# Kernel optimization log

Measured on AMD Instinct MI355X. Metric: run time of the kernel, lower is better.

Reference implementation:

```python
import jax, jax.numpy as jnp
import numpy as np

N_NODES = 100000
N_EDGES = 3200000
N_GRAPHS = 512


def setup_inputs() -> dict:
    key = jax.random.key(0)
    k1, k2, k3, k4, k5 = jax.random.split(key, 5)
    x = jax.random.normal(k1, (N_NODES, 5), dtype=jnp.float32)
    edge_index = jax.random.randint(k2, (2, N_EDGES), 0, N_NODES, dtype=jnp.int64)
    batch = jnp.sort(jax.random.randint(k3, (N_NODES,), 0, N_GRAPHS, dtype=jnp.int64))
    W1 = jax.random.normal(k4, (5, 16), dtype=jnp.float32) * (1.0 / np.sqrt(5.0))
    b1 = jnp.zeros((16,), dtype=jnp.float32)
    W2 = jax.random.normal(k5, (16, 16), dtype=jnp.float32) * 0.25
    b2 = jnp.zeros((16,), dtype=jnp.float32)
    return {"x": x, "edge_index": edge_index, "batch": batch,
            "W1": W1, "b1": b1, "W2": W2, "b2": b2}


def _gcn_conv(x, src, dst, norm, W, b, n_nodes):
    # PyG GCNConv: h = X W; out_i = sum_{j->i} norm_ij * h_j + b
    h = x @ W                                   # [N, out]
    msgs = h[src] * norm[:, None]               # gather + scale  [E_tot, out]
    out = jax.ops.segment_sum(msgs, dst, num_segments=n_nodes)
    return out + b


def reference(x, edge_index, batch, W1, b1, W2, b2):
    n = x.shape[0]
    # add self-loops (GCNConv default)
    loops = jnp.arange(n, dtype=edge_index.dtype)
    src = jnp.concatenate([edge_index[0], loops])
    dst = jnp.concatenate([edge_index[1], loops])
    # symmetric normalization: deg computed on destination nodes
    deg = jax.ops.segment_sum(jnp.ones_like(src, dtype=x.dtype), dst, num_segments=n)
    dinv = jnp.where(deg > 0, jax.lax.rsqrt(deg), 0.0)
    norm = dinv[src] * dinv[dst]                # [E_tot]

    h = jax.nn.relu(_gcn_conv(x, src, dst, norm, W1, b1, n))
    h = jax.nn.relu(_gcn_conv(h, src, dst, norm, W2, b2, n))

    # global mean pool over graphs in the batch
    sums = jax.ops.segment_sum(h, batch, num_segments=N_GRAPHS)
    cnts = jax.ops.segment_sum(jnp.ones((n,), dtype=h.dtype), batch, num_segments=N_GRAPHS)
    return sums / jnp.maximum(cnts, 1.0)[:, None]
```

## Files before the change

### kernel.cpp

```cpp
#include <hip/hip_runtime.h>

#define N_NODES  100000
#define N_EDGES  3200000
#define N_GRAPHS 512
#define F_IN     5
#define F_HID    16

#define PBLK   512
#define CHUNK  4096
#define NBLK   ((N_EDGES + CHUNK - 1) / CHUNK)
#define BKT_NODES 256
#define NBKT ((N_NODES + BKT_NODES - 1) / BKT_NODES)
#define HPAD   512
#define CAP    10240


__device__ inline unsigned short f2bf(float f) {
    unsigned u = __float_as_uint(f);
    return (unsigned short)((u + 0x7fffu + ((u >> 16) & 1u)) >> 16);
}
__device__ inline float bf2f(unsigned short h) {
    return __uint_as_float(((unsigned)h) << 16);
}
__device__ inline void unpack16(uint4 r0, uint4 r1, float* f) {
    f[0]  = bf2f((unsigned short)r0.x); f[1]  = bf2f((unsigned short)(r0.x >> 16));
    f[2]  = bf2f((unsigned short)r0.y); f[3]  = bf2f((unsigned short)(r0.y >> 16));
    f[4]  = bf2f((unsigned short)r0.z); f[5]  = bf2f((unsigned short)(r0.z >> 16));
    f[6]  = bf2f((unsigned short)r0.w); f[7]  = bf2f((unsigned short)(r0.w >> 16));
    f[8]  = bf2f((unsigned short)r1.x); f[9]  = bf2f((unsigned short)(r1.x >> 16));
    f[10] = bf2f((unsigned short)r1.y); f[11] = bf2f((unsigned short)(r1.y >> 16));
    f[12] = bf2f((unsigned short)r1.z); f[13] = bf2f((unsigned short)(r1.z >> 16));
    f[14] = bf2f((unsigned short)r1.w); f[15] = bf2f((unsigned short)(r1.w >> 16));
}

template <int NW>
__device__ inline int block_incl_scan(int v, int t, int* wsum) {
    int lane = t & 63, wave = t >> 6;
    int x = v;
#pragma unroll
    for (int o = 1; o < 64; o <<= 1) {
        int y = __shfl_up(x, o, 64);
        if (lane >= o) x += y;
    }
    if (lane == 63) wsum[wave] = x;
    __syncthreads();
    if (t < 64) {
        int w = (t < NW) ? wsum[t] : 0;
#pragma unroll
        for (int o = 1; o < NW; o <<= 1) {
            int y = __shfl_up(w, o, 64);
            if (t >= o) w += y;
        }
        if (t < NW) wsum[t] = w;
    }
    __syncthreads();
    return x + (wave ? wsum[wave - 1] : 0);
}


__global__ void k_zero(float* __restrict__ out, float* __restrict__ cnt) {
    int i = blockIdx.x * blockDim.x + threadIdx.x;
    if (i < N_GRAPHS * F_HID) out[i] = 0.0f;
    if (i < N_GRAPHS) cnt[i] = 0.0f;
}

__global__ __launch_bounds__(PBLK) void k_count(const int* __restrict__ dst,
                                                const int* __restrict__ batch,
                                                int* __restrict__ H,
                                                float* __restrict__ cnt) {
    __shared__ int hist[HPAD];
    __shared__ int bcnt[8];
    __shared__ int g0s;
    int t = threadIdx.x, blk = blockIdx.x;
    int chunk0 = blk * CHUNK;
    int n4 = min(CHUNK, N_EDGES - chunk0) >> 2;
    hist[t] = 0;
    if (t < 8) bcnt[t] = 0;
    if (t == 0 && blk < NBKT) {
        int nb = blk * BKT_NODES;
        g0s = batch[nb < N_NODES ? nb : N_NODES - 1];
    }
    __syncthreads();
    const int4* d4 = (const int4*)(dst + chunk0);
#pragma unroll
    for (int i = 0; i < CHUNK / 4 / PBLK; i++) {
        int k = t + i * PBLK;
        if (k < n4) {
            int4 d = d4[k];
            atomicAdd(&hist[d.x >> 8], 1);
            atomicAdd(&hist[d.y >> 8], 1);
            atomicAdd(&hist[d.z >> 8], 1);
            atomicAdd(&hist[d.w >> 8], 1);
        }
    }
    if (blk < NBKT && t < BKT_NODES) {
        int i2 = blk * BKT_NODES + t;
        if (i2 < N_NODES) {
            int g = batch[i2];
            int l = g - g0s;
            if (l >= 0 && l < 8) atomicAdd(&bcnt[l], 1);
            else atomicAdd(&cnt[g], 1.0f);
        }
    }
    __syncthreads();
    H[blk * HPAD + t] = hist[t];
    if (blk < NBKT && t < 8 && bcnt[t] > 0) atomicAdd(&cnt[g0s + t], (float)bcnt[t]);
}

__global__ __launch_bounds__(256) void k_scan(int* __restrict__ H,
                                              int* __restrict__ cnt_b) {
    __shared__ int wsum[8];
    int b = blockIdx.x, t = threadIdx.x;
    int v[4];
    int s = 0;
#pragma unroll
    for (int i = 0; i < 4; i++) {
        int pos = t * 4 + i;
        v[i] = (pos < NBLK) ? H[pos * HPAD + b] : 0;
        s += v[i];
    }
    int incl = block_incl_scan<4>(s, t, wsum);
    int run = incl - s;
#pragma unroll
    for (int i = 0; i < 4; i++) {
        int pos = t * 4 + i;
        if (pos < NBLK) H[pos * HPAD + b] = run;
        run += v[i];
    }
    if (t == 255) cnt_b[b] = incl;
}

__global__ __launch_bounds__(PBLK) void k_scatter(const int* __restrict__ src,
                                                  const int* __restrict__ dst,
                                                  const int* __restrict__ H,
                                                  unsigned* __restrict__ packed) {
    __shared__ int hist[HPAD];
    __shared__ int scn[HPAD];
    __shared__ int rnk[HPAD];
    __shared__ int base[HPAD];
    __shared__ int wsum[8];
    __shared__ unsigned pkd[CHUNK];
    __shared__ unsigned short bkt[CHUNK];
    int t = threadIdx.x, blk = blockIdx.x;
    int chunk0 = blk * CHUNK;
    int n = min(CHUNK, N_EDGES - chunk0);
    int n4 = n >> 2;
    hist[t] = 0;
    base[t] = H[blk * HPAD + t];
    __syncthreads();
    const int4* s4 = (const int4*)(src + chunk0);
    const int4* d4 = (const int4*)(dst + chunk0);
    int4 lsv[CHUNK / 4 / PBLK], ldv[CHUNK / 4 / PBLK];
#pragma unroll
    for (int i = 0; i < CHUNK / 4 / PBLK; i++) {
        int k = t + i * PBLK;
        if (k < n4) {
            lsv[i] = s4[k];
            ldv[i] = d4[k];
            atomicAdd(&hist[ldv[i].x >> 8], 1);
            atomicAdd(&hist[ldv[i].y >> 8], 1);
            atomicAdd(&hist[ldv[i].z >> 8], 1);
            atomicAdd(&hist[ldv[i].w >> 8], 1);
        }
    }
    __syncthreads();
    int v = hist[t];
    int incl = block_incl_scan<8>(v, t, wsum);
    int excl = incl - v;
    scn[t] = excl;
    rnk[t] = excl;
    __syncthreads();
#pragma unroll
    for (int i = 0; i < CHUNK / 4 / PBLK; i++) {
        int k = t + i * PBLK;
        if (k < n4) {
            int ds0 = ldv[i].x, ds1 = ldv[i].y, ds2 = ldv[i].z, ds3 = ldv[i].w;
            int ss0 = lsv[i].x, ss1 = lsv[i].y, ss2 = lsv[i].z, ss3 = lsv[i].w;
            int b0 = ds0 >> 8, b1 = ds1 >> 8, b2 = ds2 >> 8, b3 = ds3 >> 8;
            int r0 = atomicAdd(&rnk[b0], 1);
            pkd[r0] = ((unsigned)ss0 << 8) | (unsigned)(ds0 & 255);
            bkt[r0] = (unsigned short)b0;
            int r1 = atomicAdd(&rnk[b1], 1);
            pkd[r1] = ((unsigned)ss1 << 8) | (unsigned)(ds1 & 255);
            bkt[r1] = (unsigned short)b1;
            int r2 = atomicAdd(&rnk[b2], 1);
            pkd[r2] = ((unsigned)ss2 << 8) | (unsigned)(ds2 & 255);
            bkt[r2] = (unsigned short)b2;
            int r3 = atomicAdd(&rnk[b3], 1);
            pkd[r3] = ((unsigned)ss3 << 8) | (unsigned)(ds3 & 255);
            bkt[r3] = (unsigned short)b3;
        }
    }
    __syncthreads();
    for (int p = t; p < n; p += PBLK) {
        int b = bkt[p];
        packed[(size_t)b * CAP + base[b] + (p - scn[b])] = pkd[p];
    }
}

__global__ __launch_bounds__(1024) void k_deg(const int* __restrict__ cnt_b,
                                              const unsigned* __restrict__ packed,
                                              const float* __restrict__ x,
                                              const float* __restrict__ W1,
                                              float* __restrict__ dinv,
                                              unsigned short* __restrict__ pb) {
    __shared__ int hist[BKT_NODES];
    __shared__ float w1[F_IN * F_HID];
    __shared__ int tots;
    int b = blockIdx.x, t = threadIdx.x;
    if (t < BKT_NODES) hist[t] = 0;
    if (t >= 256 && t < 256 + F_IN * F_HID) w1[t - 256] = W1[t - 256];
    if (t == 0) tots = min(cnt_b[b], CAP);
    __syncthreads();
    int tot = tots;
    const unsigned* pk = packed + (size_t)b * CAP;
    for (int k = t; k < tot; k += 1024)
        atomicAdd(&hist[pk[k] & 255], 1);
    __syncthreads();
    if (t < BKT_NODES) {
        int node = b * BKT_NODES + t;
        if (node < N_NODES) {
            float di = rsqrtf((float)(1 + hist[t]));
            dinv[node] = di;
            float xi[F_IN];
#pragma unroll
            for (int k = 0; k < F_IN; k++) xi[k] = x[node * F_IN + k];
            unsigned pkk[8];
#pragma unroll
            for (int q = 0; q < 8; q++) {
                float h0 = 0.0f, h1 = 0.0f;
#pragma unroll
                for (int k = 0; k < F_IN; k++) {
                    h0 += xi[k] * w1[k * F_HID + 2 * q];
                    h1 += xi[k] * w1[k * F_HID + 2 * q + 1];
                }
                pkk[q] = (unsigned)f2bf(h0 * di) | ((unsigned)f2bf(h1 * di) << 16);
            }
            uint4* d4 = (uint4*)(pb + (size_t)node * F_HID);
            d4[0] = make_uint4(pkk[0], pkk[1], pkk[2], pkk[3]);
            d4[1] = make_uint4(pkk[4], pkk[5], pkk[6], pkk[7]);
        }
    }
}

__global__ __launch_bounds__(1024) void k_agg1(const int* __restrict__ cnt_b,
                                               const unsigned* __restrict__ packed,
                                               const unsigned short* __restrict__ pb,
                                               const float* __restrict__ dinv,
                                               const float* __restrict__ W2,
                                               const float* __restrict__ b1,
                                               unsigned short* __restrict__ pb2) {
    __shared__ int hist[BKT_NODES];
    __shared__ int beg[BKT_NODES];
    __shared__ int rnk[BKT_NODES];
    __shared__ int wsum[16];
    __shared__ float w2[F_HID * F_HID];
    __shared__ float b1s[F_HID];
    __shared__ int colL[CAP];
    __shared__ int tots;
    int b = blockIdx.x, t = threadIdx.x;
    const uint4* pb16 = (const uint4*)pb;
    if (t < BKT_NODES) hist[t] = 0;
    if (t >= 256 && t < 512) w2[t - 256] = W2[t - 256];
    if (t >= 512 && t < 512 + F_HID) b1s[t - 512] = b1[t - 512];
    if (t == 0) tots = min(cnt_b[b], CAP);
    __syncthreads();
    int tot = tots;
    const unsigned* pk = packed + (size_t)b * CAP;
    for (int k = t; k < tot; k += 1024)
        atomicAdd(&hist[pk[k] & 255], 1);
    __syncthreads();
    int v = (t < BKT_NODES) ? hist[t] : 0;
    int incl = block_incl_scan<16>(v, t, wsum);
    if (t < BKT_NODES) { beg[t] = incl - v; rnk[t] = incl - v; }
    __syncthreads();
    for (int k = t; k < tot; k += 1024) {
        unsigned u = pk[k];
        int r = atomicAdd(&rnk[u & 255], 1);
        colL[r] = (int)(u >> 8);
    }
    __syncthreads();
    int nl = t >> 2, q = t & 3;
    int node = b * BKT_NODES + nl;
    float f[F_HID];
    if (node < N_NODES && q == 0) {
        unpack16(pb16[node * 2], pb16[node * 2 + 1], f);
    } else {
#pragma unroll
        for (int c = 0; c < F_HID; c++) f[c] = 0.0f;
    }
    if (node < N_NODES) {
        int b0 = beg[nl], len = hist[nl];
        for (int i = q; i < len; i += 4) {
            int s = colL[b0 + i];
            uint4 r0 = pb16[s * 2], r1 = pb16[s * 2 + 1];
            float g[F_HID];
            unpack16(r0, r1, g);
#pragma unroll
            for (int c = 0; c < F_HID; c++) f[c] += g[c];
        }
    }
#pragma unroll
    for (int c = 0; c < F_HID; c++) {
        f[c] += __shfl_xor(f[c], 1, 64);
        f[c] += __shfl_xor(f[c], 2, 64);
    }
    if (node < N_NODES) {
        float di = dinv[node];
        float h[F_HID];
#pragma unroll
        for (int c = 0; c < F_HID; c++)
            h[c] = fmaxf(di * f[c] + b1s[c], 0.0f);
        float m0 = 0.0f, m1 = 0.0f, m2 = 0.0f, m3 = 0.0f;
#pragma unroll
        for (int c = 0; c < F_HID; c++) {
            float4 wv = *(const float4*)&w2[c * F_HID + 4 * q];
            m0 += h[c] * wv.x; m1 += h[c] * wv.y; m2 += h[c] * wv.z; m3 += h[c] * wv.w;
        }
        unsigned p0 = (unsigned)f2bf(m0 * di) | ((unsigned)f2bf(m1 * di) << 16);
        unsigned p1 = (unsigned)f2bf(m2 * di) | ((unsigned)f2bf(m3 * di) << 16);
        *(uint2*)(pb2 + (size_t)node * F_HID + 4 * q) = make_uint2(p0, p1);
    }
}

__global__ __launch_bounds__(1024) void k_agg2(const int* __restrict__ cnt_b,
                                               const unsigned* __restrict__ packed,
                                               const unsigned short* __restrict__ pb,
                                               const float* __restrict__ dinv,
                                               const int* __restrict__ batch,
                                               const float* __restrict__ b2,
                                               const float* __restrict__ cnt,
                                               float* __restrict__ out) {
    __shared__ int hist[BKT_NODES];
    __shared__ int beg[BKT_NODES];
    __shared__ int rnk[BKT_NODES];
    __shared__ int wsum[16];
    __shared__ float b2s[F_HID];
    __shared__ float accT[F_HID][BKT_NODES];
    __shared__ int bl[BKT_NODES];
    __shared__ int colL[CAP];
    __shared__ int tots;
    int b = blockIdx.x, t = threadIdx.x;
    const uint4* pb16 = (const uint4*)pb;
    if (t < BKT_NODES) {
        hist[t] = 0;
        int nn = b * BKT_NODES + t;
        bl[t] = (nn < N_NODES) ? batch[nn] : -1;
    }
    if (t >= 512 && t < 512 + F_HID) b2s[t - 512] = b2[t - 512];
    if (t == 0) tots = min(cnt_b[b], CAP);
    __syncthreads();
    int tot = tots;
    const unsigned* pk = packed + (size_t)b * CAP;
    for (int k = t; k < tot; k += 1024)
        atomicAdd(&hist[pk[k] & 255], 1);
    __syncthreads();
    int v = (t < BKT_NODES) ? hist[t] : 0;
    int incl = block_incl_scan<16>(v, t, wsum);
    if (t < BKT_NODES) { beg[t] = incl - v; rnk[t] = incl - v; }
    __syncthreads();
    for (int k = t; k < tot; k += 1024) {
        unsigned u = pk[k];
        int r = atomicAdd(&rnk[u & 255], 1);
        colL[r] = (int)(u >> 8);
    }
    __syncthreads();
    int nl = t >> 2, q = t & 3;
    int node = b * BKT_NODES + nl;
    float f[F_HID];
    if (node < N_NODES && q == 0) {
        unpack16(pb16[node * 2], pb16[node * 2 + 1], f);
    } else {
#pragma unroll
        for (int c = 0; c < F_HID; c++) f[c] = 0.0f;
    }
    if (node < N_NODES) {
        int b0 = beg[nl], len = hist[nl];
        for (int i = q; i < len; i += 4) {
            int s = colL[b0 + i];
            uint4 r0 = pb16[s * 2], r1 = pb16[s * 2 + 1];
            float g[F_HID];
            unpack16(r0, r1, g);
#pragma unroll
            for (int c = 0; c < F_HID; c++) f[c] += g[c];
        }
    }
#pragma unroll
    for (int c = 0; c < F_HID; c++) {
        f[c] += __shfl_xor(f[c], 1, 64);
        f[c] += __shfl_xor(f[c], 2, 64);
    }
    if (node < N_NODES) {
        float di = dinv[node];
#pragma unroll
        for (int e = 0; e < 4; e++) {
            int c = 4 * q + e;
            accT[c][nl] = fmaxf(di * f[c] + b2s[c], 0.0f);
        }
    }
    __syncthreads();
    if (t < 256) {
        int l = t >> 4, ch = t & 15;
        int g = bl[0] + l;
        if (g < N_GRAPHS) {
            float s = 0.0f;
            int m = 0;
            for (int n0 = 0; n0 < 256; n0++) {
                int n = (n0 + ch + 16 * l) & 255;
                if (bl[n] == g) { s += accT[ch][n]; m++; }
            }
            if (m > 0) atomicAdd(&out[g * F_HID + ch], s / cnt[g]);
        }
    }
}


extern "C" void kernel_launch(void* const* d_in, const int* in_sizes, int n_in,
                              void* d_out, int out_size, void* d_ws, size_t ws_size,
                              hipStream_t stream) {
    const float* x     = (const float*)d_in[0];
    const int*   ei    = (const int*)d_in[1];
    const int*   batch = (const int*)d_in[2];
    const float* W1    = (const float*)d_in[3];
    const float* b1    = (const float*)d_in[4];
    const float* W2    = (const float*)d_in[5];
    const float* b2    = (const float*)d_in[6];
    float* out = (float*)d_out;

    int*            H      = (int*)d_ws;
    int*            cnt_b  = H + (size_t)NBLK * HPAD;
    unsigned*       packed = (unsigned*)(cnt_b + 512);
    float*          dinv   = (float*)(packed + (size_t)NBKT * CAP);
    unsigned short* pb_a   = (unsigned short*)(dinv + N_NODES);
    unsigned short* pb_b   = pb_a + (size_t)N_NODES * F_HID;
    float*          cnt    = (float*)(pb_b + (size_t)N_NODES * F_HID);

    const int* src = ei;
    const int* dst = ei + N_EDGES;

    k_zero<<<(N_GRAPHS * F_HID + 255) / 256, 256, 0, stream>>>(out, cnt);
    k_count<<<NBLK, PBLK, 0, stream>>>(dst, batch, H, cnt);
    k_scan<<<NBKT, 256, 0, stream>>>(H, cnt_b);
    k_scatter<<<NBLK, PBLK, 0, stream>>>(src, dst, H, packed);
    k_deg<<<NBKT, 1024, 0, stream>>>(cnt_b, packed, x, W1, dinv, pb_a);
    k_agg1<<<NBKT, 1024, 0, stream>>>(cnt_b, packed, pb_a, dinv, W2, b1, pb_b);
    k_agg2<<<NBKT, 1024, 0, stream>>>(cnt_b, packed, pb_b, dinv, batch, b2, cnt, out);
}
```

Baseline: 187.2 us.

## Replace bucketed shared-memory sort with global-atomic CSR build and per-node pull

Replaces the two-level bucket sort (per-chunk shared histograms, transposed scan, bucket scatter, then a per-bucket local re-sort in every aggregation kernel) with a direct CSR build: global atomic degree count, three-stage scan to row offsets, and a fill pass using global atomic cursors. The aggregation kernels then read the CSR column array directly in small 256-thread blocks instead of re-sorting each bucket in shared memory twice. This removes the repeated per-layer local sort and its large shared memory footprint, but adds heavy global atomic traffic (two passes of 3.2M random atomics) and writes edges in a scattered, nondeterministic order within each row.

```diff
diff --git a/kernel.cpp b/kernel.cpp
--- a/kernel.cpp
+++ b/kernel.cpp
@@ -6,13 +6,11 @@
 #define F_IN     5
 #define F_HID    16
 
-#define PBLK   512
-#define CHUNK  4096
-#define NBLK   ((N_EDGES + CHUNK - 1) / CHUNK)
-#define BKT_NODES 256
-#define NBKT ((N_NODES + BKT_NODES - 1) / BKT_NODES)
-#define HPAD   512
-#define CAP    10240
+#define NB256  ((N_NODES + 255) / 256)
+#define EBLK   2048
+#define NEB    ((N_EDGES + EBLK - 1) / EBLK)
+#define PN     64
+#define NPB    ((N_NODES + PN - 1) / PN)
 
 
 __device__ inline unsigned short f2bf(float f) {
@@ -58,242 +56,161 @@
 }
 
 
-__global__ void k_zero(float* __restrict__ out, float* __restrict__ cnt) {
-    int i = blockIdx.x * blockDim.x + threadIdx.x;
+__global__ __launch_bounds__(256) void k_zero(int* __restrict__ deg,
+                                              float* __restrict__ out,
+                                              float* __restrict__ cnt) {
+    int i = blockIdx.x * 256 + threadIdx.x;
+    if (i < N_NODES) deg[i] = 0;
     if (i < N_GRAPHS * F_HID) out[i] = 0.0f;
     if (i < N_GRAPHS) cnt[i] = 0.0f;
 }
 
-__global__ __launch_bounds__(PBLK) void k_count(const int* __restrict__ dst,
-                                                const int* __restrict__ batch,
-                                                int* __restrict__ H,
-                                                float* __restrict__ cnt) {
-    __shared__ int hist[HPAD];
+__global__ __launch_bounds__(256) void k_deg0(const int* __restrict__ dst,
+                                              int* __restrict__ deg) {
+    int t = threadIdx.x, blk = blockIdx.x;
+    int c0 = blk * EBLK;
+    int n4 = min(EBLK, N_EDGES - c0) >> 2;
+    const int4* d4 = (const int4*)(dst + c0);
+#pragma unroll
+    for (int i = 0; i < EBLK / 4 / 256; i++) {
+        int k = t + i * 256;
+        if (k < n4) {
+            int4 d = d4[k];
+            atomicAdd(&deg[d.x], 1);
+            atomicAdd(&deg[d.y], 1);
+            atomicAdd(&deg[d.z], 1);
+            atomicAdd(&deg[d.w], 1);
+        }
+    }
+}
+
+__global__ __launch_bounds__(256) void k_scanA(const int* __restrict__ deg,
+                                               const int* __restrict__ batch,
+                                               int* __restrict__ S,
+                                               float* __restrict__ cnt) {
+    __shared__ int wsum[4];
     __shared__ int bcnt[8];
     __shared__ int g0s;
+    int b = blockIdx.x, t = threadIdx.x;
+    int node = b * 256 + t;
+    if (t < 8) bcnt[t] = 0;
+    if (t == 0) g0s = batch[(b * 256) < N_NODES ? (b * 256) : N_NODES - 1];
+    __syncthreads();
+    int v = (node < N_NODES) ? deg[node] : 0;
+    int lane = t & 63, wave = t >> 6;
+    int x = v;
+#pragma unroll
+    for (int o = 1; o < 64; o <<= 1) x += __shfl_xor(x, o, 64);
+    if (lane == 0) wsum[wave] = x;
+    if (node < N_NODES) {
+        int g = batch[node];
+        int l = g - g0s;
+        if (l >= 0 && l < 8) atomicAdd(&bcnt[l], 1);
+        else atomicAdd(&cnt[g], 1.0f);
+    }
+    __syncthreads();
+    if (t == 0) S[b] = wsum[0] + wsum[1] + wsum[2] + wsum[3];
+    if (t < 8 && bcnt[t] > 0) atomicAdd(&cnt[g0s + t], (float)bcnt[t]);
+}
+
+__global__ __launch_bounds__(512) void k_scanB(const int* __restrict__ S,
+                                               int* __restrict__ Boff) {
+    __shared__ int wsum[8];
+    int t = threadIdx.x;
+    int v = (t < NB256) ? S[t] : 0;
+    int incl = block_incl_scan<8>(v, t, wsum);
+    if (t < NB256) Boff[t] = incl - v;
+}
+
+__global__ __launch_bounds__(256) void k_scanC(const int* __restrict__ deg,
+                                               const int* __restrict__ Boff,
+                                               const float* __restrict__ x,
+                                               const float* __restrict__ W1,
+                                               int2* __restrict__ rowbc,
+                                               int* __restrict__ cur,
+                                               float* __restrict__ dinv,
+                                               unsigned short* __restrict__ pb) {
+    __shared__ int wsum[4];
+    __shared__ float w1[F_IN * F_HID];
+    int b = blockIdx.x, t = threadIdx.x;
+    if (t < F_IN * F_HID) w1[t] = W1[t];
+    int node = b * 256 + t;
+    int v = (node < N_NODES) ? deg[node] : 0;
+    int incl = block_incl_scan<4>(v, t, wsum);
+    int beg = Boff[b] + incl - v;
+    if (node < N_NODES) {
+        rowbc[node] = make_int2(beg, v);
+        cur[node] = beg;
+        float di = rsqrtf((float)(1 + v));
+        dinv[node] = di;
+        float xi[F_IN];
+#pragma unroll
+        for (int k = 0; k < F_IN; k++) xi[k] = x[node * F_IN + k];
+        unsigned pkk[8];
+#pragma unroll
+        for (int q = 0; q < 8; q++) {
+            float h0 = 0.0f, h1 = 0.0f;
+#pragma unroll
+            for (int k = 0; k < F_IN; k++) {
+                h0 += xi[k] * w1[k * F_HID + 2 * q];
+                h1 += xi[k] * w1[k * F_HID + 2 * q + 1];
+            }
+            pkk[q] = (unsigned)f2bf(h0 * di) | ((unsigned)f2bf(h1 * di) << 16);
+        }
+        uint4* d4 = (uint4*)(pb + (size_t)node * F_HID);
+        d4[0] = make_uint4(pkk[0], pkk[1], pkk[2], pkk[3]);
+        d4[1] = make_uint4(pkk[4], pkk[5], pkk[6], pkk[7]);
+    }
+}
+
+__global__ __launch_bounds__(256) void k_fill(const int* __restrict__ src,
+                                              const int* __restrict__ dst,
+                                              int* __restrict__ cur,
+                                              int* __restrict__ col) {
     int t = threadIdx.x, blk = blockIdx.x;
-    int chunk0 = blk * CHUNK;
-    int n4 = min(CHUNK, N_EDGES - chunk0) >> 2;
-    hist[t] = 0;
-    if (t < 8) bcnt[t] = 0;
-    if (t == 0 && blk < NBKT) {
-        int nb = blk * BKT_NODES;
-        g0s = batch[nb < N_NODES ? nb : N_NODES - 1];
-    }
-    __syncthreads();
-    const int4* d4 = (const int4*)(dst + chunk0);
-#pragma unroll
-    for (int i = 0; i < CHUNK / 4 / PBLK; i++) {
-        int k = t + i * PBLK;
+    int c0 = blk * EBLK;
+    int n4 = min(EBLK, N_EDGES - c0) >> 2;
+    const int4* s4 = (const int4*)(src + c0);
+    const int4* d4 = (const int4*)(dst + c0);
+#pragma unroll
+    for (int i = 0; i < EBLK / 4 / 256; i++) {
+        int k = t + i * 256;
         if (k < n4) {
-            int4 d = d4[k];
-            atomicAdd(&hist[d.x >> 8], 1);
-            atomicAdd(&hist[d.y >> 8], 1);
-            atomicAdd(&hist[d.z >> 8], 1);
-            atomicAdd(&hist[d.w >> 8], 1);
-        }
-    }
-    if (blk < NBKT && t < BKT_NODES) {
-        int i2 = blk * BKT_NODES + t;
-        if (i2 < N_NODES) {
-            int g = batch[i2];
-            int l = g - g0s;
-            if (l >= 0 && l < 8) atomicAdd(&bcnt[l], 1);
-            else atomicAdd(&cnt[g], 1.0f);
-        }
-    }
-    __syncthreads();
-    H[blk * HPAD + t] = hist[t];
-    if (blk < NBKT && t < 8 && bcnt[t] > 0) atomicAdd(&cnt[g0s + t], (float)bcnt[t]);
-}
-
-__global__ __launch_bounds__(256) void k_scan(int* __restrict__ H,
-                                              int* __restrict__ cnt_b) {
-    __shared__ int wsum[8];
-    int b = blockIdx.x, t = threadIdx.x;
-    int v[4];
-    int s = 0;
-#pragma unroll
-    for (int i = 0; i < 4; i++) {
-        int pos = t * 4 + i;
-        v[i] = (pos < NBLK) ? H[pos * HPAD + b] : 0;
-        s += v[i];
-    }
-    int incl = block_incl_scan<4>(s, t, wsum);
-    int run = incl - s;
-#pragma unroll
-    for (int i = 0; i < 4; i++) {
-        int pos = t * 4 + i;
-        if (pos < NBLK) H[pos * HPAD + b] = run;
-        run += v[i];
-    }
-    if (t == 255) cnt_b[b] = incl;
-}
-
-__global__ __launch_bounds__(PBLK) void k_scatter(const int* __restrict__ src,
-                                                  const int* __restrict__ dst,
-                                                  const int* __restrict__ H,
-                                                  unsigned* __restrict__ packed) {
-    __shared__ int hist[HPAD];
-    __shared__ int scn[HPAD];
-    __shared__ int rnk[HPAD];
-    __shared__ int base[HPAD];
-    __shared__ int wsum[8];
-    __shared__ unsigned pkd[CHUNK];
-    __shared__ unsigned short bkt[CHUNK];
-    int t = threadIdx.x, blk = blockIdx.x;
-    int chunk0 = blk * CHUNK;
-    int n = min(CHUNK, N_EDGES - chunk0);
-    int n4 = n >> 2;
-    hist[t] = 0;
-    base[t] = H[blk * HPAD + t];
-    __syncthreads();
-    const int4* s4 = (const int4*)(src + chunk0);
-    const int4* d4 = (const int4*)(dst + chunk0);
-    int4 lsv[CHUNK / 4 / PBLK], ldv[CHUNK / 4 / PBLK];
-#pragma unroll
-    for (int i = 0; i < CHUNK / 4 / PBLK; i++) {
-        int k = t + i * PBLK;
-        if (k < n4) {
-            lsv[i] = s4[k];
-            ldv[i] = d4[k];
-            atomicAdd(&hist[ldv[i].x >> 8], 1);
-            atomicAdd(&hist[ldv[i].y >> 8], 1);
-            atomicAdd(&hist[ldv[i].z >> 8], 1);
-            atomicAdd(&hist[ldv[i].w >> 8], 1);
-        }
-    }
-    __syncthreads();
-    int v = hist[t];
-    int incl = block_incl_scan<8>(v, t, wsum);
-    int excl = incl - v;
-    scn[t] = excl;
-    rnk[t] = excl;
-    __syncthreads();
-#pragma unroll
-    for (int i = 0; i < CHUNK / 4 / PBLK; i++) {
-        int k = t + i * PBLK;
-        if (k < n4) {
-            int ds0 = ldv[i].x, ds1 = ldv[i].y, ds2 = ldv[i].z, ds3 = ldv[i].w;
-            int ss0 = lsv[i].x, ss1 = lsv[i].y, ss2 = lsv[i].z, ss3 = lsv[i].w;
-            int b0 = ds0 >> 8, b1 = ds1 >> 8, b2 = ds2 >> 8, b3 = ds3 >> 8;
-            int r0 = atomicAdd(&rnk[b0], 1);
-            pkd[r0] = ((unsigned)ss0 << 8) | (unsigned)(ds0 & 255);
-            bkt[r0] = (unsigned short)b0;
-            int r1 = atomicAdd(&rnk[b1], 1);
-            pkd[r1] = ((unsigned)ss1 << 8) | (unsigned)(ds1 & 255);
-            bkt[r1] = (unsigned short)b1;
-            int r2 = atomicAdd(&rnk[b2], 1);
-            pkd[r2] = ((unsigned)ss2 << 8) | (unsigned)(ds2 & 255);
-            bkt[r2] = (unsigned short)b2;
-            int r3 = atomicAdd(&rnk[b3], 1);
-            pkd[r3] = ((unsigned)ss3 << 8) | (unsigned)(ds3 & 255);
-            bkt[r3] = (unsigned short)b3;
-        }
-    }
-    __syncthreads();
-    for (int p = t; p < n; p += PBLK) {
-        int b = bkt[p];
-        packed[(size_t)b * CAP + base[b] + (p - scn[b])] = pkd[p];
-    }
-}
-
-__global__ __launch_bounds__(1024) void k_deg(const int* __restrict__ cnt_b,
-                                              const unsigned* __restrict__ packed,
-                                              const float* __restrict__ x,
-                                              const float* __restrict__ W1,
-                                              float* __restrict__ dinv,
-                                              unsigned short* __restrict__ pb) {
-    __shared__ int hist[BKT_NODES];
-    __shared__ float w1[F_IN * F_HID];
-    __shared__ int tots;
-    int b = blockIdx.x, t = threadIdx.x;
-    if (t < BKT_NODES) hist[t] = 0;
-    if (t >= 256 && t < 256 + F_IN * F_HID) w1[t - 256] = W1[t - 256];
-    if (t == 0) tots = min(cnt_b[b], CAP);
-    __syncthreads();
-    int tot = tots;
-    const unsigned* pk = packed + (size_t)b * CAP;
-    for (int k = t; k < tot; k += 1024)
-        atomicAdd(&hist[pk[k] & 255], 1);
-    __syncthreads();
-    if (t < BKT_NODES) {
-        int node = b * BKT_NODES + t;
-        if (node < N_NODES) {
-            float di = rsqrtf((float)(1 + hist[t]));
-            dinv[node] = di;
-            float xi[F_IN];
-#pragma unroll
-            for (int k = 0; k < F_IN; k++) xi[k] = x[node * F_IN + k];
-            unsigned pkk[8];
-#pragma unroll
-            for (int q = 0; q < 8; q++) {
-                float h0 = 0.0f, h1 = 0.0f;
-#pragma unroll
-                for (int k = 0; k < F_IN; k++) {
-                    h0 += xi[k] * w1[k * F_HID + 2 * q];
-                    h1 += xi[k] * w1[k * F_HID + 2 * q + 1];
-                }
-                pkk[q] = (unsigned)f2bf(h0 * di) | ((unsigned)f2bf(h1 * di) << 16);
-            }
-            uint4* d4 = (uint4*)(pb + (size_t)node * F_HID);
-            d4[0] = make_uint4(pkk[0], pkk[1], pkk[2], pkk[3]);
-            d4[1] = make_uint4(pkk[4], pkk[5], pkk[6], pkk[7]);
-        }
-    }
-}
-
-__global__ __launch_bounds__(1024) void k_agg1(const int* __restrict__ cnt_b,
-                                               const unsigned* __restrict__ packed,
+            int4 s = s4[k], d = d4[k];
+            int r0 = atomicAdd(&cur[d.x], 1); col[r0] = s.x;
+            int r1 = atomicAdd(&cur[d.y], 1); col[r1] = s.y;
+            int r2 = atomicAdd(&cur[d.z], 1); col[r2] = s.z;
+            int r3 = atomicAdd(&cur[d.w], 1); col[r3] = s.w;
+        }
+    }
+}
+
+__global__ __launch_bounds__(256) void k_pull1(const int2* __restrict__ rowbc,
+                                               const int* __restrict__ col,
                                                const unsigned short* __restrict__ pb,
                                                const float* __restrict__ dinv,
                                                const float* __restrict__ W2,
                                                const float* __restrict__ b1,
                                                unsigned short* __restrict__ pb2) {
-    __shared__ int hist[BKT_NODES];
-    __shared__ int beg[BKT_NODES];
-    __shared__ int rnk[BKT_NODES];
-    __shared__ int wsum[16];
     __shared__ float w2[F_HID * F_HID];
     __shared__ float b1s[F_HID];
-    __shared__ int colL[CAP];
-    __shared__ int tots;
-    int b = blockIdx.x, t = threadIdx.x;
+    int t = threadIdx.x;
+    w2[t] = W2[t];
+    if (t < F_HID) b1s[t] = b1[t];
+    __syncthreads();
+    int nl = t >> 2, q = t & 3;
+    int node = blockIdx.x * PN + nl;
     const uint4* pb16 = (const uint4*)pb;
-    if (t < BKT_NODES) hist[t] = 0;
-    if (t >= 256 && t < 512) w2[t - 256] = W2[t - 256];
-    if (t >= 512 && t < 512 + F_HID) b1s[t - 512] = b1[t - 512];
-    if (t == 0) tots = min(cnt_b[b], CAP);
-    __syncthreads();
-    int tot = tots;
-    const unsigned* pk = packed + (size_t)b * CAP;
-    for (int k = t; k < tot; k += 1024)
-        atomicAdd(&hist[pk[k] & 255], 1);
-    __syncthreads();
-    int v = (t < BKT_NODES) ? hist[t] : 0;
-    int incl = block_incl_scan<16>(v, t, wsum);
-    if (t < BKT_NODES) { beg[t] = incl - v; rnk[t] = incl - v; }
-    __syncthreads();
-    for (int k = t; k < tot; k += 1024) {
-        unsigned u = pk[k];
-        int r = atomicAdd(&rnk[u & 255], 1);
-        colL[r] = (int)(u >> 8);
-    }
-    __syncthreads();
-    int nl = t >> 2, q = t & 3;
-    int node = b * BKT_NODES + nl;
     float f[F_HID];
-    if (node < N_NODES && q == 0) {
-        unpack16(pb16[node * 2], pb16[node * 2 + 1], f);
-    } else {
-#pragma unroll
-        for (int c = 0; c < F_HID; c++) f[c] = 0.0f;
-    }
-    if (node < N_NODES) {
-        int b0 = beg[nl], len = hist[nl];
-        for (int i = q; i < len; i += 4) {
-            int s = colL[b0 + i];
-            uint4 r0 = pb16[s * 2], r1 = pb16[s * 2 + 1];
+#pragma unroll
+    for (int c = 0; c < F_HID; c++) f[c] = 0.0f;
+    int2 rc = make_int2(0, 0);
+    if (node < N_NODES) {
+        rc = rowbc[node];
+        if (q == 0) unpack16(pb16[2 * node], pb16[2 * node + 1], f);
+        for (int i = q; i < rc.y; i += 4) {
+            int s = col[rc.x + i];
+            uint4 r0 = pb16[2 * s], r1 = pb16[2 * s + 1];
             float g[F_HID];
             unpack16(r0, r1, g);
 #pragma unroll
@@ -323,62 +240,36 @@
     }
 }
 
-__global__ __launch_bounds__(1024) void k_agg2(const int* __restrict__ cnt_b,
-                                               const unsigned* __restrict__ packed,
+__global__ __launch_bounds__(256) void k_pull2(const int2* __restrict__ rowbc,
+                                               const int* __restrict__ col,
                                                const unsigned short* __restrict__ pb,
                                                const float* __restrict__ dinv,
                                                const int* __restrict__ batch,
                                                const float* __restrict__ b2,
                                                const float* __restrict__ cnt,
                                                float* __restrict__ out) {
-    __shared__ int hist[BKT_NODES];
-    __shared__ int beg[BKT_NODES];
-    __shared__ int rnk[BKT_NODES];
-    __shared__ int wsum[16];
     __shared__ float b2s[F_HID];
-    __shared__ float accT[F_HID][BKT_NODES];
-    __shared__ int bl[BKT_NODES];
-    __shared__ int colL[CAP];
-    __shared__ int tots;
-    int b = blockIdx.x, t = threadIdx.x;
+    __shared__ float hbuf[PN][F_HID + 1];
+    __shared__ int bl[PN];
+    int t = threadIdx.x;
+    if (t < F_HID) b2s[t] = b2[t];
+    if (t < PN) {
+        int nn = blockIdx.x * PN + t;
+        bl[t] = (nn < N_NODES) ? batch[nn] : -1;
+    }
+    __syncthreads();
+    int nl = t >> 2, q = t & 3;
+    int node = blockIdx.x * PN + nl;
     const uint4* pb16 = (const uint4*)pb;
-    if (t < BKT_NODES) {
-        hist[t] = 0;
-        int nn = b * BKT_NODES + t;
-        bl[t] = (nn < N_NODES) ? batch[nn] : -1;
-    }
-    if (t >= 512 && t < 512 + F_HID) b2s[t - 512] = b2[t - 512];
-    if (t == 0) tots = min(cnt_b[b], CAP);
-    __syncthreads();
-    int tot = tots;
-    const unsigned* pk = packed + (size_t)b * CAP;
-    for (int k = t; k < tot; k += 1024)
-        atomicAdd(&hist[pk[k] & 255], 1);
-    __syncthreads();
-    int v = (t < BKT_NODES) ? hist[t] : 0;
-    int incl = block_incl_scan<16>(v, t, wsum);
-    if (t < BKT_NODES) { beg[t] = incl - v; rnk[t] = incl - v; }
-    __syncthreads();
-    for (int k = t; k < tot; k += 1024) {
-        unsigned u = pk[k];
-        int r = atomicAdd(&rnk[u & 255], 1);
-        colL[r] = (int)(u >> 8);
-    }
-    __syncthreads();
-    int nl = t >> 2, q = t & 3;
-    int node = b * BKT_NODES + nl;
     float f[F_HID];
-    if (node < N_NODES && q == 0) {
-        unpack16(pb16[node * 2], pb16[node * 2 + 1], f);
-    } else {
-#pragma unroll
-        for (int c = 0; c < F_HID; c++) f[c] = 0.0f;
-    }
-    if (node < N_NODES) {
-        int b0 = beg[nl], len = hist[nl];
-        for (int i = q; i < len; i += 4) {
-            int s = colL[b0 + i];
-            uint4 r0 = pb16[s * 2], r1 = pb16[s * 2 + 1];
+#pragma unroll
+    for (int c = 0; c < F_HID; c++) f[c] = 0.0f;
+    if (node < N_NODES) {
+        int2 rc = rowbc[node];
+        if (q == 0) unpack16(pb16[2 * node], pb16[2 * node + 1], f);
+        for (int i = q; i < rc.y; i += 4) {
+            int s = col[rc.x + i];
+            uint4 r0 = pb16[2 * s], r1 = pb16[2 * s + 1];
             float g[F_HID];
             unpack16(r0, r1, g);
 #pragma unroll
@@ -390,24 +281,22 @@
         f[c] += __shfl_xor(f[c], 1, 64);
         f[c] += __shfl_xor(f[c], 2, 64);
     }
-    if (node < N_NODES) {
+    if (node < N_NODES && q == 0) {
         float di = dinv[node];
 #pragma unroll
-        for (int e = 0; e < 4; e++) {
-            int c = 4 * q + e;
-            accT[c][nl] = fmaxf(di * f[c] + b2s[c], 0.0f);
-        }
-    }
-    __syncthreads();
-    if (t < 256) {
+        for (int c = 0; c < F_HID; c++)
+            hbuf[nl][c] = fmaxf(di * f[c] + b2s[c], 0.0f);
+    }
+    __syncthreads();
+    if (t < 8 * F_HID) {
         int l = t >> 4, ch = t & 15;
         int g = bl[0] + l;
         if (g < N_GRAPHS) {
             float s = 0.0f;
             int m = 0;
-            for (int n0 = 0; n0 < 256; n0++) {
-                int n = (n0 + ch + 16 * l) & 255;
-                if (bl[n] == g) { s += accT[ch][n]; m++; }
+            for (int n0 = 0; n0 < PN; n0++) {
+                int n = (n0 + (ch << 2)) & (PN - 1);
+                if (bl[n] == g) { s += hbuf[n][ch]; m++; }
             }
             if (m > 0) atomicAdd(&out[g * F_HID + ch], s / cnt[g]);
         }
@@ -427,22 +316,26 @@
     const float* b2    = (const float*)d_in[6];
     float* out = (float*)d_out;
 
-    int*            H      = (int*)d_ws;
-    int*            cnt_b  = H + (size_t)NBLK * HPAD;
-    unsigned*       packed = (unsigned*)(cnt_b + 512);
-    float*          dinv   = (float*)(packed + (size_t)NBKT * CAP);
-    unsigned short* pb_a   = (unsigned short*)(dinv + N_NODES);
-    unsigned short* pb_b   = pb_a + (size_t)N_NODES * F_HID;
-    float*          cnt    = (float*)(pb_b + (size_t)N_NODES * F_HID);
+    int*            deg   = (int*)d_ws;
+    int*            S     = deg + N_NODES;
+    int*            Boff  = S + 512;
+    int*            cur   = Boff + 512;
+    int2*           rowbc = (int2*)(cur + N_NODES);
+    int*            col   = (int*)(rowbc + N_NODES);
+    float*          dinv  = (float*)(col + (size_t)N_EDGES);
+    unsigned short* pb_a  = (unsigned short*)(dinv + N_NODES);
+    unsigned short* pb_b  = pb_a + (size_t)N_NODES * F_HID;
+    float*          cnt   = (float*)(pb_b + (size_t)N_NODES * F_HID);
 
     const int* src = ei;
     const int* dst = ei + N_EDGES;
 
-    k_zero<<<(N_GRAPHS * F_HID + 255) / 256, 256, 0, stream>>>(out, cnt);
-    k_count<<<NBLK, PBLK, 0, stream>>>(dst, batch, H, cnt);
-    k_scan<<<NBKT, 256, 0, stream>>>(H, cnt_b);
-    k_scatter<<<NBLK, PBLK, 0, stream>>>(src, dst, H, packed);
-    k_deg<<<NBKT, 1024, 0, stream>>>(cnt_b, packed, x, W1, dinv, pb_a);
-    k_agg1<<<NBKT, 1024, 0, stream>>>(cnt_b, packed, pb_a, dinv, W2, b1, pb_b);
-    k_agg2<<<NBKT, 1024, 0, stream>>>(cnt_b, packed, pb_b, dinv, batch, b2, cnt, out);
-}
+    k_zero <<<NB256, 256, 0, stream>>>(deg, out, cnt);
+    k_deg0 <<<NEB,   256, 0, stream>>>(dst, deg);
+    k_scanA<<<NB256, 256, 0, stream>>>(deg, batch, S, cnt);
+    k_scanB<<<1,     512, 0, stream>>>(S, Boff);
+    k_scanC<<<NB256, 256, 0, stream>>>(deg, Boff, x, W1, rowbc, cur, dinv, pb_a);
+    k_fill <<<NEB,   256, 0, stream>>>(src, dst, cur, col);
+    k_pull1<<<NPB,   256, 0, stream>>>(rowbc, col, pb_a, dinv, W2, b1, pb_b);
+    k_pull2<<<NPB,   256, 0, stream>>>(rowbc, col, pb_b, dinv, batch, b2, cnt, out);
+}
```

Result: slower. 528.2 us (+182.2%).

## Build global CSR once and use small-block pull kernels for aggregation

Applied to the files above, without the earlier changes.

The per-bucket local sort of packed edges now runs once in k_csr, which writes a global CSR (row begin/count plus column array). The two aggregation kernels then become small 256-thread pull kernels over 64 nodes each, with no per-kernel histogram, scan or sort. k_scatter reuses a copy of the per-chunk histogram saved by k_count instead of recomputing it, so the edge chunk is read only once there. The cost is extra global writes and reads for the col array and the histogram copy, plus smaller pooling blocks that issue more atomics to the output.

```diff
diff --git a/kernel.cpp b/kernel.cpp
--- a/kernel.cpp
+++ b/kernel.cpp
@@ -13,6 +13,8 @@
 #define NBKT ((N_NODES + BKT_NODES - 1) / BKT_NODES)
 #define HPAD   512
 #define CAP    10240
+#define PN     64
+#define NPB    ((N_NODES + PN - 1) / PN)
 
 
 __device__ inline unsigned short f2bf(float f) {
@@ -58,8 +60,9 @@
 }
 
 
-__global__ void k_zero(float* __restrict__ out, float* __restrict__ cnt) {
-    int i = blockIdx.x * blockDim.x + threadIdx.x;
+__global__ __launch_bounds__(256) void k_zero(float* __restrict__ out,
+                                              float* __restrict__ cnt) {
+    int i = blockIdx.x * 256 + threadIdx.x;
     if (i < N_GRAPHS * F_HID) out[i] = 0.0f;
     if (i < N_GRAPHS) cnt[i] = 0.0f;
 }
@@ -67,6 +70,7 @@
 __global__ __launch_bounds__(PBLK) void k_count(const int* __restrict__ dst,
                                                 const int* __restrict__ batch,
                                                 int* __restrict__ H,
+                                                int* __restrict__ Hc,
                                                 float* __restrict__ cnt) {
     __shared__ int hist[HPAD];
     __shared__ int bcnt[8];
@@ -103,7 +107,9 @@
         }
     }
     __syncthreads();
-    H[blk * HPAD + t] = hist[t];
+    int v = hist[t];
+    H[blk * HPAD + t] = v;
+    Hc[blk * HPAD + t] = v;
     if (blk < NBKT && t < 8 && bcnt[t] > 0) atomicAdd(&cnt[g0s + t], (float)bcnt[t]);
 }
 
@@ -133,8 +139,8 @@
 __global__ __launch_bounds__(PBLK) void k_scatter(const int* __restrict__ src,
                                                   const int* __restrict__ dst,
                                                   const int* __restrict__ H,
+                                                  const int* __restrict__ Hc,
                                                   unsigned* __restrict__ packed) {
-    __shared__ int hist[HPAD];
     __shared__ int scn[HPAD];
     __shared__ int rnk[HPAD];
     __shared__ int base[HPAD];
@@ -145,49 +151,32 @@
     int chunk0 = blk * CHUNK;
     int n = min(CHUNK, N_EDGES - chunk0);
     int n4 = n >> 2;
-    hist[t] = 0;
     base[t] = H[blk * HPAD + t];
-    __syncthreads();
-    const int4* s4 = (const int4*)(src + chunk0);
-    const int4* d4 = (const int4*)(dst + chunk0);
-    int4 lsv[CHUNK / 4 / PBLK], ldv[CHUNK / 4 / PBLK];
-#pragma unroll
-    for (int i = 0; i < CHUNK / 4 / PBLK; i++) {
-        int k = t + i * PBLK;
-        if (k < n4) {
-            lsv[i] = s4[k];
-            ldv[i] = d4[k];
-            atomicAdd(&hist[ldv[i].x >> 8], 1);
-            atomicAdd(&hist[ldv[i].y >> 8], 1);
-            atomicAdd(&hist[ldv[i].z >> 8], 1);
-            atomicAdd(&hist[ldv[i].w >> 8], 1);
-        }
-    }
-    __syncthreads();
-    int v = hist[t];
+    int v = Hc[blk * HPAD + t];
     int incl = block_incl_scan<8>(v, t, wsum);
     int excl = incl - v;
     scn[t] = excl;
     rnk[t] = excl;
     __syncthreads();
+    const int4* s4 = (const int4*)(src + chunk0);
+    const int4* d4 = (const int4*)(dst + chunk0);
 #pragma unroll
     for (int i = 0; i < CHUNK / 4 / PBLK; i++) {
         int k = t + i * PBLK;
         if (k < n4) {
-            int ds0 = ldv[i].x, ds1 = ldv[i].y, ds2 = ldv[i].z, ds3 = ldv[i].w;
-            int ss0 = lsv[i].x, ss1 = lsv[i].y, ss2 = lsv[i].z, ss3 = lsv[i].w;
-            int b0 = ds0 >> 8, b1 = ds1 >> 8, b2 = ds2 >> 8, b3 = ds3 >> 8;
+            int4 s = s4[k], d = d4[k];
+            int b0 = d.x >> 8, b1 = d.y >> 8, b2 = d.z >> 8, b3 = d.w >> 8;
             int r0 = atomicAdd(&rnk[b0], 1);
-            pkd[r0] = ((unsigned)ss0 << 8) | (unsigned)(ds0 & 255);
+            pkd[r0] = ((unsigned)s.x << 8) | (unsigned)(d.x & 255);
             bkt[r0] = (unsigned short)b0;
             int r1 = atomicAdd(&rnk[b1], 1);
-            pkd[r1] = ((unsigned)ss1 << 8) | (unsigned)(ds1 & 255);
+            pkd[r1] = ((unsigned)s.y << 8) | (unsigned)(d.y & 255);
             bkt[r1] = (unsigned short)b1;
             int r2 = atomicAdd(&rnk[b2], 1);
-            pkd[r2] = ((unsigned)ss2 << 8) | (unsigned)(ds2 & 255);
+            pkd[r2] = ((unsigned)s.z << 8) | (unsigned)(d.z & 255);
             bkt[r2] = (unsigned short)b2;
             int r3 = atomicAdd(&rnk[b3], 1);
-            pkd[r3] = ((unsigned)ss3 << 8) | (unsigned)(ds3 & 255);
+            pkd[r3] = ((unsigned)s.w << 8) | (unsigned)(d.w & 255);
             bkt[r3] = (unsigned short)b3;
         }
     }
@@ -198,29 +187,49 @@
     }
 }
 
-__global__ __launch_bounds__(1024) void k_deg(const int* __restrict__ cnt_b,
-                                              const unsigned* __restrict__ packed,
-                                              const float* __restrict__ x,
-                                              const float* __restrict__ W1,
-                                              float* __restrict__ dinv,
-                                              unsigned short* __restrict__ pb) {
+__global__ __launch_bounds__(512) void k_csr(const int* __restrict__ cnt_b,
+                                             const unsigned* __restrict__ packed,
+                                             const float* __restrict__ x,
+                                             const float* __restrict__ W1,
+                                             int2* __restrict__ rowbc,
+                                             int* __restrict__ col,
+                                             float* __restrict__ dinv,
+                                             unsigned short* __restrict__ pb) {
     __shared__ int hist[BKT_NODES];
+    __shared__ int beg[BKT_NODES];
+    __shared__ int rnk2[BKT_NODES];
+    __shared__ int wsum[8];
     __shared__ float w1[F_IN * F_HID];
+    __shared__ unsigned pkd[CAP];
     __shared__ int tots;
     int b = blockIdx.x, t = threadIdx.x;
+    int gbase = b * CAP;
     if (t < BKT_NODES) hist[t] = 0;
-    if (t >= 256 && t < 256 + F_IN * F_HID) w1[t - 256] = W1[t - 256];
     if (t == 0) tots = min(cnt_b[b], CAP);
+    if (t >= 512 - F_IN * F_HID) w1[t - (512 - F_IN * F_HID)] = W1[t - (512 - F_IN * F_HID)];
     __syncthreads();
     int tot = tots;
     const unsigned* pk = packed + (size_t)b * CAP;
-    for (int k = t; k < tot; k += 1024)
-        atomicAdd(&hist[pk[k] & 255], 1);
-    __syncthreads();
+    for (int k = t; k < tot; k += 512) {
+        unsigned u = pk[k];
+        pkd[k] = u;
+        atomicAdd(&hist[u & 255], 1);
+    }
+    __syncthreads();
+    int v = (t < BKT_NODES) ? hist[t] : 0;
+    int incl = block_incl_scan<8>(v, t, wsum);
+    if (t < BKT_NODES) { beg[t] = incl - v; rnk2[t] = incl - v; }
+    __syncthreads();
+    for (int e = t; e < tot; e += 512) {
+        unsigned w = pkd[e];
+        int r = atomicAdd(&rnk2[w & 255], 1);
+        col[gbase + r] = (int)(w >> 8);
+    }
     if (t < BKT_NODES) {
         int node = b * BKT_NODES + t;
         if (node < N_NODES) {
-            float di = rsqrtf((float)(1 + hist[t]));
+            rowbc[node] = make_int2(gbase + beg[t], v);
+            float di = rsqrtf((float)(1 + v));
             dinv[node] = di;
             float xi[F_IN];
 #pragma unroll
@@ -243,57 +252,31 @@
     }
 }
 
-__global__ __launch_bounds__(1024) void k_agg1(const int* __restrict__ cnt_b,
-                                               const unsigned* __restrict__ packed,
+__global__ __launch_bounds__(256) void k_pull1(const int2* __restrict__ rowbc,
+                                               const int* __restrict__ col,
                                                const unsigned short* __restrict__ pb,
                                                const float* __restrict__ dinv,
                                                const float* __restrict__ W2,
                                                const float* __restrict__ b1,
                                                unsigned short* __restrict__ pb2) {
-    __shared__ int hist[BKT_NODES];
-    __shared__ int beg[BKT_NODES];
-    __shared__ int rnk[BKT_NODES];
-    __shared__ int wsum[16];
     __shared__ float w2[F_HID * F_HID];
     __shared__ float b1s[F_HID];
-    __shared__ int colL[CAP];
-    __shared__ int tots;
-    int b = blockIdx.x, t = threadIdx.x;
+    int t = threadIdx.x;
+    w2[t] = W2[t];
+    if (t < F_HID) b1s[t] = b1[t];
+    __syncthreads();
+    int nl = t >> 2, q = t & 3;
+    int node = blockIdx.x * PN + nl;
     const uint4* pb16 = (const uint4*)pb;
-    if (t < BKT_NODES) hist[t] = 0;
-    if (t >= 256 && t < 512) w2[t - 256] = W2[t - 256];
-    if (t >= 512 && t < 512 + F_HID) b1s[t - 512] = b1[t - 512];
-    if (t == 0) tots = min(cnt_b[b], CAP);
-    __syncthreads();
-    int tot = tots;
-    const unsigned* pk = packed + (size_t)b * CAP;
-    for (int k = t; k < tot; k += 1024)
-        atomicAdd(&hist[pk[k] & 255], 1);
-    __syncthreads();
-    int v = (t < BKT_NODES) ? hist[t] : 0;
-    int incl = block_incl_scan<16>(v, t, wsum);
-    if (t < BKT_NODES) { beg[t] = incl - v; rnk[t] = incl - v; }
-    __syncthreads();
-    for (int k = t; k < tot; k += 1024) {
-        unsigned u = pk[k];
-        int r = atomicAdd(&rnk[u & 255], 1);
-        colL[r] = (int)(u >> 8);
-    }
-    __syncthreads();
-    int nl = t >> 2, q = t & 3;
-    int node = b * BKT_NODES + nl;
     float f[F_HID];
-    if (node < N_NODES && q == 0) {
-        unpack16(pb16[node * 2], pb16[node * 2 + 1], f);
-    } else {
-#pragma unroll
-        for (int c = 0; c < F_HID; c++) f[c] = 0.0f;
-    }
+#pragma unroll
+    for (int c = 0; c < F_HID; c++) f[c] = 0.0f;
     if (node < N_NODES) {
-        int b0 = beg[nl], len = hist[nl];
-        for (int i = q; i < len; i += 4) {
-            int s = colL[b0 + i];
-            uint4 r0 = pb16[s * 2], r1 = pb16[s * 2 + 1];
+        int2 rc = rowbc[node];
+        if (q == 0) unpack16(pb16[2 * node], pb16[2 * node + 1], f);
+        for (int i = q; i < rc.y; i += 4) {
+            int s = col[rc.x + i];
+            uint4 r0 = pb16[2 * s], r1 = pb16[2 * s + 1];
             float g[F_HID];
             unpack16(r0, r1, g);
 #pragma unroll
@@ -323,62 +306,36 @@
     }
 }
 
-__global__ __launch_bounds__(1024) void k_agg2(const int* __restrict__ cnt_b,
-                                               const unsigned* __restrict__ packed,
+__global__ __launch_bounds__(256) void k_pull2(const int2* __restrict__ rowbc,
+                                               const int* __restrict__ col,
                                                const unsigned short* __restrict__ pb,
                                                const float* __restrict__ dinv,
                                                const int* __restrict__ batch,
                                                const float* __restrict__ b2,
                                                const float* __restrict__ cnt,
                                                float* __restrict__ out) {
-    __shared__ int hist[BKT_NODES];
-    __shared__ int beg[BKT_NODES];
-    __shared__ int rnk[BKT_NODES];
-    __shared__ int wsum[16];
     __shared__ float b2s[F_HID];
-    __shared__ float accT[F_HID][BKT_NODES];
-    __shared__ int bl[BKT_NODES];
-    __shared__ int colL[CAP];
-    __shared__ int tots;
-    int b = blockIdx.x, t = threadIdx.x;
+    __shared__ float hbuf[PN][F_HID + 1];
+    __shared__ int bl[PN];
+    int t = threadIdx.x;
+    if (t < F_HID) b2s[t] = b2[t];
+    if (t < PN) {
+        int nn = blockIdx.x * PN + t;
+        bl[t] = (nn < N_NODES) ? batch[nn] : -1;
+    }
+    __syncthreads();
+    int nl = t >> 2, q = t & 3;
+    int node = blockIdx.x * PN + nl;
     const uint4* pb16 = (const uint4*)pb;
-    if (t < BKT_NODES) {
-        hist[t] = 0;
-        int nn = b * BKT_NODES + t;
-        bl[t] = (nn < N_NODES) ? batch[nn] : -1;
-    }
-    if (t >= 512 && t < 512 + F_HID) b2s[t - 512] = b2[t - 512];
-    if (t == 0) tots = min(cnt_b[b], CAP);
-    __syncthreads();
-    int tot = tots;
-    const unsigned* pk = packed + (size_t)b * CAP;
-    for (int k = t; k < tot; k += 1024)
-        atomicAdd(&hist[pk[k] & 255], 1);
-    __syncthreads();
-    int v = (t < BKT_NODES) ? hist[t] : 0;
-    int incl = block_incl_scan<16>(v, t, wsum);
-    if (t < BKT_NODES) { beg[t] = incl - v; rnk[t] = incl - v; }
-    __syncthreads();
-    for (int k = t; k < tot; k += 1024) {
-        unsigned u = pk[k];
-        int r = atomicAdd(&rnk[u & 255], 1);
-        colL[r] = (int)(u >> 8);
-    }
-    __syncthreads();
-    int nl = t >> 2, q = t & 3;
-    int node = b * BKT_NODES + nl;
     float f[F_HID];
-    if (node < N_NODES && q == 0) {
-        unpack16(pb16[node * 2], pb16[node * 2 + 1], f);
-    } else {
-#pragma unroll
-        for (int c = 0; c < F_HID; c++) f[c] = 0.0f;
-    }
+#pragma unroll
+    for (int c = 0; c < F_HID; c++) f[c] = 0.0f;
     if (node < N_NODES) {
-        int b0 = beg[nl], len = hist[nl];
-        for (int i = q; i < len; i += 4) {
-            int s = colL[b0 + i];
-            uint4 r0 = pb16[s * 2], r1 = pb16[s * 2 + 1];
+        int2 rc = rowbc[node];
+        if (q == 0) unpack16(pb16[2 * node], pb16[2 * node + 1], f);
+        for (int i = q; i < rc.y; i += 4) {
+            int s = col[rc.x + i];
+            uint4 r0 = pb16[2 * s], r1 = pb16[2 * s + 1];
             float g[F_HID];
             unpack16(r0, r1, g);
 #pragma unroll
@@ -390,24 +347,22 @@
         f[c] += __shfl_xor(f[c], 1, 64);
         f[c] += __shfl_xor(f[c], 2, 64);
     }
-    if (node < N_NODES) {
+    if (node < N_NODES && q == 0) {
         float di = dinv[node];
 #pragma unroll
-        for (int e = 0; e < 4; e++) {
-            int c = 4 * q + e;
-            accT[c][nl] = fmaxf(di * f[c] + b2s[c], 0.0f);
-        }
-    }
-    __syncthreads();
-    if (t < 256) {
+        for (int c = 0; c < F_HID; c++)
+            hbuf[nl][c] = fmaxf(di * f[c] + b2s[c], 0.0f);
+    }
+    __syncthreads();
+    if (t < 8 * F_HID) {
         int l = t >> 4, ch = t & 15;
         int g = bl[0] + l;
         if (g < N_GRAPHS) {
             float s = 0.0f;
             int m = 0;
-            for (int n0 = 0; n0 < 256; n0++) {
-                int n = (n0 + ch + 16 * l) & 255;
-                if (bl[n] == g) { s += accT[ch][n]; m++; }
+            for (int n0 = 0; n0 < PN; n0++) {
+                int n = (n0 + (ch << 2)) & (PN - 1);
+                if (bl[n] == g) { s += hbuf[n][ch]; m++; }
             }
             if (m > 0) atomicAdd(&out[g * F_HID + ch], s / cnt[g]);
         }
@@ -428,9 +383,12 @@
     float* out = (float*)d_out;
 
     int*            H      = (int*)d_ws;
-    int*            cnt_b  = H + (size_t)NBLK * HPAD;
+    int*            Hc     = H + (size_t)NBLK * HPAD;
+    int*            cnt_b  = Hc + (size_t)NBLK * HPAD;
     unsigned*       packed = (unsigned*)(cnt_b + 512);
-    float*          dinv   = (float*)(packed + (size_t)NBKT * CAP);
+    int2*           rowbc  = (int2*)(packed + (size_t)NBKT * CAP);
+    int*            col    = (int*)(rowbc + N_NODES);
+    float*          dinv   = (float*)(col + (size_t)NBKT * CAP);
     unsigned short* pb_a   = (unsigned short*)(dinv + N_NODES);
     unsigned short* pb_b   = pb_a + (size_t)N_NODES * F_HID;
     float*          cnt    = (float*)(pb_b + (size_t)N_NODES * F_HID);
@@ -438,11 +396,11 @@
     const int* src = ei;
     const int* dst = ei + N_EDGES;
 
-    k_zero<<<(N_GRAPHS * F_HID + 255) / 256, 256, 0, stream>>>(out, cnt);
-    k_count<<<NBLK, PBLK, 0, stream>>>(dst, batch, H, cnt);
-    k_scan<<<NBKT, 256, 0, stream>>>(H, cnt_b);
-    k_scatter<<<NBLK, PBLK, 0, stream>>>(src, dst, H, packed);
-    k_deg<<<NBKT, 1024, 0, stream>>>(cnt_b, packed, x, W1, dinv, pb_a);
-    k_agg1<<<NBKT, 1024, 0, stream>>>(cnt_b, packed, pb_a, dinv, W2, b1, pb_b);
-    k_agg2<<<NBKT, 1024, 0, stream>>>(cnt_b, packed, pb_b, dinv, batch, b2, cnt, out);
-}
+    k_zero   <<<(N_GRAPHS * F_HID + 255) / 256, 256, 0, stream>>>(out, cnt);
+    k_count  <<<NBLK, PBLK, 0, stream>>>(dst, batch, H, Hc, cnt);
+    k_scan   <<<NBKT, 256, 0, stream>>>(H, cnt_b);
+    k_scatter<<<NBLK, PBLK, 0, stream>>>(src, dst, H, Hc, packed);
+    k_csr    <<<NBKT, 512, 0, stream>>>(cnt_b, packed, x, W1, rowbc, col, dinv, pb_a);
+    k_pull1  <<<NPB, 256, 0, stream>>>(rowbc, col, pb_a, dinv, W2, b1, pb_b);
+    k_pull2  <<<NPB, 256, 0, stream>>>(rowbc, col, pb_b, dinv, batch, b2, cnt, out);
+}
```

After: 196.7 us. 5.1% more time.
